# Optimization experiments

Hardware: AMD Instinct MI355X
Metric: run time of the kernel (lower is better)

The kernel has to match this reference:

```python
import jax, jax.numpy as jnp
import numpy as np

DIM = 96
DIM_OUT = 96
NUM_HEADS = 1
HEAD_DIM = DIM_OUT // NUM_HEADS  # 96, also depthwise-conv channel count
STRIDE_Q = 1
STRIDE_KV = 2
EPS = 1e-6


def _layernorm(t, g, b):
    mu = jnp.mean(t, axis=-1, keepdims=True)
    var = jnp.mean(jnp.square(t - mu), axis=-1, keepdims=True)
    return (t - mu) * jax.lax.rsqrt(var + EPS) * g + b


def _depthwise(t_nchw, w, stride):
    # torch Conv2d(C, C, 3, stride, padding=1, groups=C, bias=False)
    # w: [C, 1, 3, 3]
    return jax.lax.conv_general_dilated(
        t_nchw, w, window_strides=(stride, stride), padding=[(1, 1), (1, 1)],
        feature_group_count=HEAD_DIM, dimension_numbers=('NCHW', 'OIHW', 'NCHW'))


def _attention_pool(t, w, stride, g, b, H, W):
    # t: [B, heads, L, C] -> pooled [B, heads, Lp, C]
    B, nh, L, C = t.shape
    t = t.reshape(B * nh, H, W, C).transpose(0, 3, 1, 2)  # [B*nh, C, H, W]
    t = _depthwise(t, w, stride)
    Hp, Wp = t.shape[2], t.shape[3]
    t = t.reshape(B, nh, C, Hp * Wp).transpose(0, 1, 3, 2)  # [B, nh, Lp, C]
    return _layernorm(t, g, b), Hp, Wp


def setup_inputs() -> dict:
    key = jax.random.key(0)
    ks = jax.random.split(key, 16)
    B, N = 32, 56 * 56
    inp = {
        'x': jax.random.normal(ks[0], (B, N, DIM), dtype=jnp.float32),
        'Wqkv': jax.random.normal(ks[1], (3 * DIM_OUT, DIM), dtype=jnp.float32) * 0.02,
        'bqkv': jax.random.normal(ks[2], (3 * DIM_OUT,), dtype=jnp.float32) * 0.02,
        'pool_q_w': jax.random.normal(ks[3], (HEAD_DIM, 1, 3, 3), dtype=jnp.float32) * 0.1,
        'gq': 1.0 + jax.random.normal(ks[4], (HEAD_DIM,), dtype=jnp.float32) * 0.02,
        'betq': jax.random.normal(ks[5], (HEAD_DIM,), dtype=jnp.float32) * 0.02,
        'pool_k_w': jax.random.normal(ks[6], (HEAD_DIM, 1, 3, 3), dtype=jnp.float32) * 0.1,
        'gk': 1.0 + jax.random.normal(ks[7], (HEAD_DIM,), dtype=jnp.float32) * 0.02,
        'betk': jax.random.normal(ks[8], (HEAD_DIM,), dtype=jnp.float32) * 0.02,
        'pool_v_w': jax.random.normal(ks[9], (HEAD_DIM, 1, 3, 3), dtype=jnp.float32) * 0.1,
        'gv': 1.0 + jax.random.normal(ks[10], (HEAD_DIM,), dtype=jnp.float32) * 0.02,
        'betv': jax.random.normal(ks[11], (HEAD_DIM,), dtype=jnp.float32) * 0.02,
        'Wproj': jax.random.normal(ks[12], (DIM_OUT, DIM_OUT), dtype=jnp.float32) * 0.02,
        'bproj': jax.random.normal(ks[13], (DIM_OUT,), dtype=jnp.float32) * 0.02,
        'h': 56,
        'w': 56,
    }
    return inp


def reference(x, Wqkv, bqkv, pool_q_w, gq, betq, pool_k_w, gk, betk,
              pool_v_w, gv, betv, Wproj, bproj, h, w):
    B, N, _ = x.shape
    qkv = (jnp.einsum('bnd,ed->bne', x, Wqkv) + bqkv)
    qkv = qkv.reshape(B, N, 3, NUM_HEADS, HEAD_DIM).transpose(2, 0, 3, 1, 4)
    q, k, v = qkv[0], qkv[1], qkv[2]  # each [B, heads, N, head_dim]

    q, Hq, Wq = _attention_pool(q, pool_q_w, STRIDE_Q, gq, betq, h, w)
    k, _, _ = _attention_pool(k, pool_k_w, STRIDE_KV, gk, betk, h, w)
    v, _, _ = _attention_pool(v, pool_v_w, STRIDE_KV, gv, betv, h, w)

    scale = HEAD_DIM ** -0.5
    attn = jax.nn.softmax(jnp.einsum('bhqc,bhkc->bhqk', q * scale, k), axis=-1)
    out = jnp.einsum('bhqk,bhkc->bhqc', attn, v) + q  # residual x + q
    out = out.transpose(0, 2, 1, 3).reshape(B, Hq * Wq, DIM_OUT)
    out = jnp.einsum('bnd,ed->bne', out, Wproj) + bproj
    return out
```

## Files before the change

kernel.cpp:

```cpp
#include <hip/hip_runtime.h>
#include <hip/hip_bf16.h>
#include <cmath>

#define BATCH 32
#define H_IN 56
#define W_IN 56
#define N_IN (H_IN * W_IN)
#define LKV 784
#define LKV_PAD 864
#define FRAG_ELEMS 82944

typedef short bf16x8 __attribute__((ext_vector_type(8)));
typedef float f32x4 __attribute__((ext_vector_type(4)));
typedef float f32x16 __attribute__((ext_vector_type(16)));

__device__ __forceinline__ unsigned pack_bf16(float a, float b) {
    unsigned ua = __builtin_bit_cast(unsigned, a);
    unsigned ub = __builtin_bit_cast(unsigned, b);
    ua = (ua + 0x7FFFu + ((ua >> 16) & 1u)) >> 16;
    ub = (ub + 0x7FFFu + ((ub >> 16) & 1u)) >> 16;
    return ua | (ub << 16);
}

__device__ __forceinline__ unsigned short cvt_bf16(float a) {
    unsigned ua = __builtin_bit_cast(unsigned, a);
    return (unsigned short)((ua + 0x7FFFu + ((ua >> 16) & 1u)) >> 16);
}

__device__ __forceinline__ float bf16_to_f32(unsigned short u) {
    unsigned v = ((unsigned)u) << 16;
    return __builtin_bit_cast(float, v);
}

__device__ __forceinline__ float bflo(unsigned u) {
    return __builtin_bit_cast(float, u << 16);
}
__device__ __forceinline__ float bfhi(unsigned u) {
    return __builtin_bit_cast(float, u & 0xFFFF0000u);
}

__device__ __forceinline__ unsigned pack_trunc(float a, float b) {
    return __builtin_amdgcn_perm(__builtin_bit_cast(unsigned, b),
                                 __builtin_bit_cast(unsigned, a), 0x07060302u);
}

__device__ __forceinline__ f32x16 zero16() {
    f32x16 z;
#pragma unroll
    for (int i = 0; i < 16; ++i) z[i] = 0.f;
    return z;
}

__global__ __launch_bounds__(256) void wprep_kernel(
    const float* __restrict__ Wqkv, const float* __restrict__ Wproj,
    const float* __restrict__ pqw, const float* __restrict__ pkw,
    const float* __restrict__ pvw,
    unsigned short* __restrict__ wq, unsigned short* __restrict__ wp,
    float* __restrict__ wpool)
{
    int idx = blockIdx.x * 256 + threadIdx.x;
    if (idx < 4608) {
        const float* src; unsigned short* dst; int li;
        if (idx < 3456) { src = Wqkv; dst = wq; li = idx; }
        else            { src = Wproj; dst = wp; li = idx - 3456; }
        int frag = li >> 6, ln = li & 63;
        int ct = frag / 3, kkb = frag % 3;
        int ch = ct * 16 + (ln & 15);
        int k0 = kkb * 32 + (ln >> 4) * 8;
        const float* s = src + ch * 96 + k0;
        float4 v0 = *reinterpret_cast<const float4*>(s);
        float4 v1 = *reinterpret_cast<const float4*>(s + 4);
        uint4 o;
        o.x = pack_bf16(v0.x, v0.y); o.y = pack_bf16(v0.z, v0.w);
        o.z = pack_bf16(v1.x, v1.y); o.w = pack_bf16(v1.z, v1.w);
        *reinterpret_cast<uint4*>(dst + (size_t)li * 8) = o;
    } else if (idx < 7200) {
        int li = idx - 4608;
        int which = li / 864, r = li % 864;
        int tap = r / 96, c = r % 96;
        const float* src = (which == 0) ? pqw : (which == 1 ? pkw : pvw);
        wpool[which * 864 + tap * 96 + c] = src[c * 9 + tap];
    }
}

template <int NCT, bool IN_BF16, bool OUT_F32>
__global__ __launch_bounds__(256, 2) void gemm2_kernel(
    const void* __restrict__ Xv, const unsigned short* __restrict__ Wfr,
    const float* __restrict__ bias, void* __restrict__ o0,
    void* __restrict__ o1, void* __restrict__ o2)
{
    __shared__ unsigned short Wl[NCT * 192 * 8];
    const int tid = threadIdx.x;
    const int wid = tid >> 6, lane = tid & 63;
    const int lo16 = lane & 15, hi = lane >> 4;

    for (int idx = tid; idx < NCT * 192; idx += 256)
        *reinterpret_cast<int4*>(&Wl[idx * 8]) =
            *reinterpret_cast<const int4*>(Wfr + (size_t)idx * 8);

    const size_t tok0 = (size_t)blockIdx.x * 256 + wid * 64;
    bf16x8 xb[12];
#pragma unroll
    for (int it = 0; it < 4; ++it) {
        size_t t = tok0 + it * 16 + lo16;
#pragma unroll
        for (int kkb = 0; kkb < 3; ++kkb) {
            if constexpr (IN_BF16) {
                xb[it * 3 + kkb] = *reinterpret_cast<const bf16x8*>(
                    (const unsigned short*)Xv + t * 96 + kkb * 32 + hi * 8);
            } else {
                const float* xp = (const float*)Xv + t * 96 + kkb * 32 + hi * 8;
                float4 a = *reinterpret_cast<const float4*>(xp);
                float4 c = *reinterpret_cast<const float4*>(xp + 4);
                uint4 u;
                u.x = pack_bf16(a.x, a.y); u.y = pack_bf16(a.z, a.w);
                u.z = pack_bf16(c.x, c.y); u.w = pack_bf16(c.z, c.w);
                xb[it * 3 + kkb] = __builtin_bit_cast(bf16x8, u);
            }
        }
    }
    __syncthreads();

#pragma unroll
    for (int ct = 0; ct < NCT; ++ct) {
        bf16x8 wf[3];
#pragma unroll
        for (int kkb = 0; kkb < 3; ++kkb)
            wf[kkb] = *reinterpret_cast<const bf16x8*>(&Wl[((ct * 3 + kkb) * 64 + lane) * 8]);
        const int chb = ct * 16 + hi * 4;
        float4 bv = *reinterpret_cast<const float4*>(bias + chb);
#pragma unroll
        for (int it = 0; it < 4; ++it) {
            f32x4 a = (f32x4){0.f, 0.f, 0.f, 0.f};
#pragma unroll
            for (int kkb = 0; kkb < 3; ++kkb)
                a = __builtin_amdgcn_mfma_f32_16x16x32_bf16(wf[kkb], xb[it * 3 + kkb], a, 0, 0, 0);
            size_t t = tok0 + it * 16 + lo16;
            float r0 = a[0] + bv.x, r1 = a[1] + bv.y;
            float r2 = a[2] + bv.z, r3 = a[3] + bv.w;
            if constexpr (OUT_F32) {
                *reinterpret_cast<float4*>((float*)o0 + t * 96 + chb) =
                    make_float4(r0, r1, r2, r3);
            } else {
                unsigned short* ob =
                    (unsigned short*)((ct < 6) ? o0 : (ct < 12 ? o1 : o2));
                int lch = (ct % 6) * 16 + hi * 4;
                uint2 p;
                p.x = pack_bf16(r0, r1);
                p.y = pack_bf16(r2, r3);
                *reinterpret_cast<uint2*>(ob + t * 96 + lch) = p;
            }
        }
    }
}

template <int OMODE, int STRIDE>
__global__ __launch_bounds__(192) void pool_ln4_kernel(
    const unsigned short* __restrict__ in, const float* __restrict__ pwt,
    const float* __restrict__ g, const float* __restrict__ beta,
    unsigned short* __restrict__ out, int Hp, int Wp, int LpPad, float oscale)
{
    __shared__ float2 part[192];
    __shared__ float2 mrs[16];
    const int tid = threadIdx.x;
    const int tok_l = tid / 12, c8 = tid % 12;
    const int gt = blockIdx.x * 16 + tok_l;
    const int Lp = Hp * Wp;
    const int b = gt / LpPad, rem = gt % LpPad;
    const bool pad = (rem >= Lp);
    const int yo = rem / Wp, xo = rem % Wp;

    float wt[9][8];
#pragma unroll
    for (int tap = 0; tap < 9; ++tap) {
        float4 w0 = *reinterpret_cast<const float4*>(pwt + tap * 96 + c8 * 8);
        float4 w1 = *reinterpret_cast<const float4*>(pwt + tap * 96 + c8 * 8 + 4);
        wt[tap][0] = w0.x; wt[tap][1] = w0.y; wt[tap][2] = w0.z; wt[tap][3] = w0.w;
        wt[tap][4] = w1.x; wt[tap][5] = w1.y; wt[tap][6] = w1.z; wt[tap][7] = w1.w;
    }

    float acc[8];
#pragma unroll
    for (int j = 0; j < 8; ++j) acc[j] = 0.f;

    const unsigned short* ib = in + (size_t)b * (H_IN * W_IN * 96) + c8 * 8;
#pragma unroll
    for (int dy = 0; dy < 3; ++dy) {
        const int iy = yo * STRIDE + dy - 1;
        if ((unsigned)iy < (unsigned)H_IN) {
#pragma unroll
            for (int dx = 0; dx < 3; ++dx) {
                const int ix = xo * STRIDE + dx - 1;
                if ((unsigned)ix < (unsigned)W_IN) {
                    const int tap = dy * 3 + dx;
                    uint4 d = *reinterpret_cast<const uint4*>(
                        ib + ((size_t)iy * W_IN + ix) * 96);
                    acc[0] += bflo(d.x) * wt[tap][0];
                    acc[1] += bfhi(d.x) * wt[tap][1];
                    acc[2] += bflo(d.y) * wt[tap][2];
                    acc[3] += bfhi(d.y) * wt[tap][3];
                    acc[4] += bflo(d.z) * wt[tap][4];
                    acc[5] += bfhi(d.z) * wt[tap][5];
                    acc[6] += bflo(d.w) * wt[tap][6];
                    acc[7] += bfhi(d.w) * wt[tap][7];
                }
            }
        }
    }

    float s = 0.f, s2 = 0.f;
#pragma unroll
    for (int j = 0; j < 8; ++j) { s += acc[j]; s2 += acc[j] * acc[j]; }
    part[tid] = make_float2(s, s2);
    __syncthreads();
    if (tid < 16) {
        float a = 0.f, q = 0.f;
#pragma unroll
        for (int j = 0; j < 12; ++j) {
            float2 p = part[tid * 12 + j];
            a += p.x; q += p.y;
        }
        float mu = a * (1.f / 96.f);
        float var = q * (1.f / 96.f) - mu * mu;
        mrs[tid] = make_float2(mu, rsqrtf(var + 1e-6f));
    }
    __syncthreads();
    const float mu = mrs[tok_l].x, rstd = mrs[tok_l].y;

    float4 g0 = *reinterpret_cast<const float4*>(g + c8 * 8);
    float4 g1 = *reinterpret_cast<const float4*>(g + c8 * 8 + 4);
    float4 b0 = *reinterpret_cast<const float4*>(beta + c8 * 8);
    float4 b1 = *reinterpret_cast<const float4*>(beta + c8 * 8 + 4);
    float r[8];
    r[0] = (acc[0] - mu) * rstd * (g0.x * oscale) + b0.x * oscale;
    r[1] = (acc[1] - mu) * rstd * (g0.y * oscale) + b0.y * oscale;
    r[2] = (acc[2] - mu) * rstd * (g0.z * oscale) + b0.z * oscale;
    r[3] = (acc[3] - mu) * rstd * (g0.w * oscale) + b0.w * oscale;
    r[4] = (acc[4] - mu) * rstd * (g1.x * oscale) + b1.x * oscale;
    r[5] = (acc[5] - mu) * rstd * (g1.y * oscale) + b1.y * oscale;
    r[6] = (acc[6] - mu) * rstd * (g1.z * oscale) + b1.z * oscale;
    r[7] = (acc[7] - mu) * rstd * (g1.w * oscale) + b1.w * oscale;
    if (OMODE != 0 && pad) {
#pragma unroll
        for (int j = 0; j < 8; ++j) r[j] = 0.f;
    }

    if constexpr (OMODE == 0) {
        uint4 o;
        o.x = pack_bf16(r[0], r[1]); o.y = pack_bf16(r[2], r[3]);
        o.z = pack_bf16(r[4], r[5]); o.w = pack_bf16(r[6], r[7]);
        *reinterpret_cast<uint4*>(out + (size_t)gt * 96 + c8 * 8) = o;
    } else if constexpr (OMODE == 1) {
        int t = rem >> 5, kkb = c8 >> 1, hi = c8 & 1;
        int ln = (rem & 31) | (hi << 5);
        uint4 o;
        o.x = pack_bf16(r[0], r[1]); o.y = pack_bf16(r[2], r[3]);
        o.z = pack_bf16(r[4], r[5]); o.w = pack_bf16(r[6], r[7]);
        *reinterpret_cast<uint4*>(out + (size_t)b * FRAG_ELEMS +
                                  ((size_t)(t * 6 + kkb) * 64 + ln) * 8) = o;
    } else {
        int kv16 = rem >> 4, e = rem & 7, lh = (rem >> 3) & 1;
#pragma unroll
        for (int j = 0; j < 8; ++j) {
            int j8 = c8 * 8 + j;
            int ct = j8 >> 5;
            int ln = (j8 & 31) | (lh << 5);
            out[(size_t)b * FRAG_ELEMS + ((size_t)(kv16 * 3 + ct) * 64 + ln) * 8 + e] =
                cvt_bf16(r[j]);
        }
    }
}

#define ATT_LOAD(KF, V0, V1, T)                                               \
    {                                                                         \
        _Pragma("unroll") for (int i_ = 0; i_ < 6; ++i_)                      \
            KF[i_] = *reinterpret_cast<const bf16x8*>(                        \
                Kb + ((size_t)((T) * 6 + i_) * 64 + lane) * 8);               \
        _Pragma("unroll") for (int c_ = 0; c_ < 3; ++c_) {                    \
            V0[c_] = *reinterpret_cast<const bf16x8*>(                        \
                Vb + ((size_t)((2 * (T)) * 3 + c_) * 64 + lane) * 8);         \
            V1[c_] = *reinterpret_cast<const bf16x8*>(                        \
                Vb + ((size_t)((2 * (T) + 1) * 3 + c_) * 64 + lane) * 8);     \
        }                                                                     \
    }

#define ATT_COMPUTE(KF, V0, V1, FULL)                                         \
    {                                                                         \
        f32x16 s = zero16();                                                  \
        _Pragma("unroll") for (int k_ = 0; k_ < 6; ++k_)                      \
            s = __builtin_amdgcn_mfma_f32_32x32x16_bf16(KF[k_], qf[k_], s, 0, 0, 0); \
        float p[16];                                                          \
        _Pragma("unroll") for (int r_ = 0; r_ < 16; ++r_) {                   \
            float e_ = __builtin_amdgcn_exp2f(s[r_]);                         \
            p[r_] = __builtin_bit_cast(float,                                 \
                      __builtin_bit_cast(unsigned, e_) & 0xFFFF0000u);        \
        }                                                                     \
        float q0_ = 0.f, q1_ = 0.f;                                           \
        _Pragma("unroll") for (int r_ = 0; r_ < 8; ++r_) {                    \
            q0_ += p[r_]; q1_ += p[r_ + 8];                                   \
        }                                                                     \
        lsum += q0_ + ((FULL) ? q1_ : 0.f);                                   \
        unsigned d[8], sw[8];                                                 \
        _Pragma("unroll") for (int j_ = 0; j_ < 8; ++j_)                      \
            d[j_] = pack_trunc(p[2 * j_], p[2 * j_ + 1]);                     \
        _Pragma("unroll") for (int j_ = 0; j_ < 8; ++j_)                      \
            sw[j_] = (unsigned)__shfl_xor((int)d[j_], 32);                    \
        {                                                                     \
            int4 bi = h ? make_int4((int)sw[2], (int)sw[3], (int)d[2], (int)d[3]) \
                        : make_int4((int)d[0], (int)d[1], (int)sw[0], (int)sw[1]); \
            bf16x8 bf = __builtin_bit_cast(bf16x8, bi);                       \
            a0 = __builtin_amdgcn_mfma_f32_32x32x16_bf16(V0[0], bf, a0, 0, 0, 0); \
            a1 = __builtin_amdgcn_mfma_f32_32x32x16_bf16(V0[1], bf, a1, 0, 0, 0); \
            a2 = __builtin_amdgcn_mfma_f32_32x32x16_bf16(V0[2], bf, a2, 0, 0, 0); \
        }                                                                     \
        if (FULL) {                                                           \
            int4 bi = h ? make_int4((int)sw[6], (int)sw[7], (int)d[6], (int)d[7]) \
                        : make_int4((int)d[4], (int)d[5], (int)sw[4], (int)sw[5]); \
            bf16x8 bf = __builtin_bit_cast(bf16x8, bi);                       \
            a0 = __builtin_amdgcn_mfma_f32_32x32x16_bf16(V1[0], bf, a0, 0, 0, 0); \
            a1 = __builtin_amdgcn_mfma_f32_32x32x16_bf16(V1[1], bf, a1, 0, 0, 0); \
            a2 = __builtin_amdgcn_mfma_f32_32x32x16_bf16(V1[2], bf, a2, 0, 0, 0); \
        }                                                                     \
    }

__global__ __launch_bounds__(64) void attn_mfma7_kernel(
    const unsigned short* __restrict__ qpl, const unsigned short* __restrict__ Kf,
    const unsigned short* __restrict__ Vf, unsigned short* __restrict__ out)
{
    const int bid = blockIdx.x;
    const int swz = (bid & 7) * 392 + (bid >> 3);
    const int b = swz / 98, qblk = swz % 98;
    const int lane = threadIdx.x;
    const int l31 = lane & 31, h = lane >> 5;

    const int qrow = qblk * 32 + l31;
    const unsigned short* qptr = qpl + ((size_t)b * N_IN + qrow) * 96;
    bf16x8 qf[6];
#pragma unroll
    for (int kkb = 0; kkb < 6; ++kkb)
        qf[kkb] = *reinterpret_cast<const bf16x8*>(qptr + kkb * 16 + h * 8);

    f32x16 a0 = zero16(), a1 = zero16(), a2 = zero16();
    float lsum = 0.f;

    const unsigned short* Kb = Kf + (size_t)b * FRAG_ELEMS;
    const unsigned short* Vb = Vf + (size_t)b * FRAG_ELEMS;

    bf16x8 kA[6], vA0[3], vA1[3];
    bf16x8 kB[6], vB0[3], vB1[3];

    ATT_LOAD(kA, vA0, vA1, 0);
    for (int t = 0; t < 24; t += 2) {
        ATT_LOAD(kB, vB0, vB1, t + 1);
        ATT_COMPUTE(kA, vA0, vA1, true);
        ATT_LOAD(kA, vA0, vA1, t + 2);
        ATT_COMPUTE(kB, vB0, vB1, true);
    }
    ATT_COMPUTE(kA, vA0, vA1, false);

    lsum += __shfl_xor(lsum, 32);
    const float inv = 1.f / lsum;

    unsigned short* op = out + ((size_t)b * N_IN + qrow) * 96;
#pragma unroll
    for (int ct = 0; ct < 3; ++ct) {
        const f32x16& a = (ct == 0) ? a0 : (ct == 1 ? a1 : a2);
#pragma unroll
        for (int gblk = 0; gblk < 4; ++gblk) {
            int ch = ct * 32 + gblk * 8 + 4 * h;
            ushort4 q4 = *reinterpret_cast<const ushort4*>(qptr + ch);
            uint2 pr;
            pr.x = pack_bf16(a[gblk * 4 + 0] * inv + bf16_to_f32(q4.x),
                             a[gblk * 4 + 1] * inv + bf16_to_f32(q4.y));
            pr.y = pack_bf16(a[gblk * 4 + 2] * inv + bf16_to_f32(q4.z),
                             a[gblk * 4 + 3] * inv + bf16_to_f32(q4.w));
            *reinterpret_cast<uint2*>(op + ch) = pr;
        }
    }
}

extern "C" void kernel_launch(void* const* d_in, const int* in_sizes, int n_in,
                              void* d_out, int out_size, void* d_ws, size_t ws_size,
                              hipStream_t stream)
{
    const float* x     = (const float*)d_in[0];
    const float* Wqkv  = (const float*)d_in[1];
    const float* bqkv  = (const float*)d_in[2];
    const float* pqw   = (const float*)d_in[3];
    const float* gq    = (const float*)d_in[4];
    const float* betq  = (const float*)d_in[5];
    const float* pkw   = (const float*)d_in[6];
    const float* gk    = (const float*)d_in[7];
    const float* betk  = (const float*)d_in[8];
    const float* pvw   = (const float*)d_in[9];
    const float* gv    = (const float*)d_in[10];
    const float* betv  = (const float*)d_in[11];
    const float* Wproj = (const float*)d_in[12];
    const float* bproj = (const float*)d_in[13];
    float* outp = (float*)d_out;

    char* ws = (char*)d_ws;
    const size_t QB    = (size_t)BATCH * N_IN * 96 * sizeof(short);
    const size_t FRAGB = (size_t)BATCH * FRAG_ELEMS * sizeof(short);
    unsigned short* qb   = (unsigned short*)(ws);
    unsigned short* kbuf = (unsigned short*)(ws + QB);
    unsigned short* vbuf = (unsigned short*)(ws + 2 * QB);
    unsigned short* qpb  = (unsigned short*)(ws + 3 * QB);
    unsigned short* Kfr  = (unsigned short*)(ws + 4 * QB);
    unsigned short* Vfr  = (unsigned short*)(ws + 4 * QB + FRAGB);
    unsigned short* wqf  = (unsigned short*)(ws + 4 * QB + 2 * FRAGB);
    unsigned short* wpf  = (unsigned short*)(ws + 4 * QB + 2 * FRAGB + 56320);
    float*          wpool = (float*)(ws + 4 * QB + 2 * FRAGB + 56320 + 18432);
    unsigned short* attn_out = qb;

    const int T = BATCH * N_IN;

    const float SC = 0.1020620726159658f * 1.4426950408889634f;

    wprep_kernel<<<29, 256, 0, stream>>>(Wqkv, Wproj, pqw, pkw, pvw, wqf, wpf, wpool);
    gemm2_kernel<18, false, false><<<T / 256, 256, 0, stream>>>(
        x, wqf, bqkv, qb, kbuf, vbuf);
    pool_ln4_kernel<0, 1><<<T / 16, 192, 0, stream>>>(
        qb, wpool, gq, betq, qpb, 56, 56, N_IN, 1.0f);
    pool_ln4_kernel<1, 2><<<(BATCH * LKV_PAD) / 16, 192, 0, stream>>>(
        kbuf, wpool + 864, gk, betk, Kfr, 28, 28, LKV_PAD, SC);
    pool_ln4_kernel<2, 2><<<(BATCH * LKV_PAD) / 16, 192, 0, stream>>>(
        vbuf, wpool + 1728, gv, betv, Vfr, 28, 28, LKV_PAD, 1.0f);
    attn_mfma7_kernel<<<3136, 64, 0, stream>>>(qpb, Kfr, Vfr, attn_out);
    gemm2_kernel<6, true, true><<<T / 256, 256, 0, stream>>>(
        attn_out, wpf, bproj, outp, nullptr, nullptr);
}
```

Before: 151.0 us.

## Fold weight prep into GEMMs, merge pooling launches, regroup attention into 4-wave blocks

```diff
diff --git a/kernel.cpp b/kernel.cpp
--- a/kernel.cpp
+++ b/kernel.cpp
@@ -51,41 +51,9 @@
     return z;
 }
 
-__global__ __launch_bounds__(256) void wprep_kernel(
-    const float* __restrict__ Wqkv, const float* __restrict__ Wproj,
-    const float* __restrict__ pqw, const float* __restrict__ pkw,
-    const float* __restrict__ pvw,
-    unsigned short* __restrict__ wq, unsigned short* __restrict__ wp,
-    float* __restrict__ wpool)
-{
-    int idx = blockIdx.x * 256 + threadIdx.x;
-    if (idx < 4608) {
-        const float* src; unsigned short* dst; int li;
-        if (idx < 3456) { src = Wqkv; dst = wq; li = idx; }
-        else            { src = Wproj; dst = wp; li = idx - 3456; }
-        int frag = li >> 6, ln = li & 63;
-        int ct = frag / 3, kkb = frag % 3;
-        int ch = ct * 16 + (ln & 15);
-        int k0 = kkb * 32 + (ln >> 4) * 8;
-        const float* s = src + ch * 96 + k0;
-        float4 v0 = *reinterpret_cast<const float4*>(s);
-        float4 v1 = *reinterpret_cast<const float4*>(s + 4);
-        uint4 o;
-        o.x = pack_bf16(v0.x, v0.y); o.y = pack_bf16(v0.z, v0.w);
-        o.z = pack_bf16(v1.x, v1.y); o.w = pack_bf16(v1.z, v1.w);
-        *reinterpret_cast<uint4*>(dst + (size_t)li * 8) = o;
-    } else if (idx < 7200) {
-        int li = idx - 4608;
-        int which = li / 864, r = li % 864;
-        int tap = r / 96, c = r % 96;
-        const float* src = (which == 0) ? pqw : (which == 1 ? pkw : pvw);
-        wpool[which * 864 + tap * 96 + c] = src[c * 9 + tap];
-    }
-}
-
 template <int NCT, bool IN_BF16, bool OUT_F32>
-__global__ __launch_bounds__(256, 2) void gemm2_kernel(
-    const void* __restrict__ Xv, const unsigned short* __restrict__ Wfr,
+__global__ __launch_bounds__(256, 2) void gemm3_kernel(
+    const void* __restrict__ Xv, const float* __restrict__ W,
     const float* __restrict__ bias, void* __restrict__ o0,
     void* __restrict__ o1, void* __restrict__ o2)
 {
@@ -94,14 +62,24 @@
     const int wid = tid >> 6, lane = tid & 63;
     const int lo16 = lane & 15, hi = lane >> 4;
 
-    for (int idx = tid; idx < NCT * 192; idx += 256)
-        *reinterpret_cast<int4*>(&Wl[idx * 8]) =
-            *reinterpret_cast<const int4*>(Wfr + (size_t)idx * 8);
-
-    const size_t tok0 = (size_t)blockIdx.x * 256 + wid * 64;
-    bf16x8 xb[12];
-#pragma unroll
-    for (int it = 0; it < 4; ++it) {
+    for (int idx = tid; idx < NCT * 192; idx += 256) {
+        int frag = idx >> 6, ln = idx & 63;
+        int ct = frag / 3, kkb = frag % 3;
+        int ch = ct * 16 + (ln & 15);
+        int k0 = kkb * 32 + (ln >> 4) * 8;
+        const float* s = W + ch * 96 + k0;
+        float4 v0 = *reinterpret_cast<const float4*>(s);
+        float4 v1 = *reinterpret_cast<const float4*>(s + 4);
+        uint4 o;
+        o.x = pack_bf16(v0.x, v0.y); o.y = pack_bf16(v0.z, v0.w);
+        o.z = pack_bf16(v1.x, v1.y); o.w = pack_bf16(v1.z, v1.w);
+        *reinterpret_cast<uint4*>(&Wl[idx * 8]) = o;
+    }
+
+    const size_t tok0 = (size_t)blockIdx.x * 128 + wid * 32;
+    bf16x8 xb[6];
+#pragma unroll
+    for (int it = 0; it < 2; ++it) {
         size_t t = tok0 + it * 16 + lo16;
 #pragma unroll
         for (int kkb = 0; kkb < 3; ++kkb) {
@@ -130,7 +108,7 @@
         const int chb = ct * 16 + hi * 4;
         float4 bv = *reinterpret_cast<const float4*>(bias + chb);
 #pragma unroll
-        for (int it = 0; it < 4; ++it) {
+        for (int it = 0; it < 2; ++it) {
             f32x4 a = (f32x4){0.f, 0.f, 0.f, 0.f};
 #pragma unroll
             for (int kkb = 0; kkb < 3; ++kkb)
@@ -154,29 +132,56 @@
     }
 }
 
-template <int OMODE, int STRIDE>
-__global__ __launch_bounds__(192) void pool_ln4_kernel(
-    const unsigned short* __restrict__ in, const float* __restrict__ pwt,
-    const float* __restrict__ g, const float* __restrict__ beta,
-    unsigned short* __restrict__ out, int Hp, int Wp, int LpPad, float oscale)
+__global__ __launch_bounds__(192) void pool_all_kernel(
+    const unsigned short* __restrict__ qin, const unsigned short* __restrict__ kin,
+    const unsigned short* __restrict__ vin,
+    const float* __restrict__ pqw, const float* __restrict__ pkw,
+    const float* __restrict__ pvw,
+    const float* __restrict__ gq, const float* __restrict__ betq,
+    const float* __restrict__ gk, const float* __restrict__ betk,
+    const float* __restrict__ gv, const float* __restrict__ betv,
+    unsigned short* __restrict__ qout, unsigned short* __restrict__ kfr,
+    unsigned short* __restrict__ vfr, float SC)
 {
+    __shared__ float wlds[864];
     __shared__ float2 part[192];
     __shared__ float2 mrs[16];
+
+    int blk = blockIdx.x;
+    const unsigned short* in; const float* wsrc; const float* g; const float* beta;
+    unsigned short* out; int omode, stride, Wp, LpPad; float oscale;
+    if (blk < 6272) {
+        in = qin; wsrc = pqw; g = gq; beta = betq; out = qout;
+        omode = 0; stride = 1; Wp = 56; LpPad = N_IN; oscale = 1.0f;
+    } else if (blk < 8000) {
+        blk -= 6272;
+        in = kin; wsrc = pkw; g = gk; beta = betk; out = kfr;
+        omode = 1; stride = 2; Wp = 28; LpPad = LKV_PAD; oscale = SC;
+    } else {
+        blk -= 8000;
+        in = vin; wsrc = pvw; g = gv; beta = betv; out = vfr;
+        omode = 2; stride = 2; Wp = 28; LpPad = LKV_PAD; oscale = 1.0f;
+    }
+
     const int tid = threadIdx.x;
+    for (int i = tid; i < 216; i += 192)
+        *reinterpret_cast<float4*>(&wlds[i * 4]) =
+            *reinterpret_cast<const float4*>(wsrc + i * 4);
+    __syncthreads();
+
     const int tok_l = tid / 12, c8 = tid % 12;
-    const int gt = blockIdx.x * 16 + tok_l;
-    const int Lp = Hp * Wp;
+    const int gt = blk * 16 + tok_l;
+    const int Lp = (omode == 0) ? N_IN : LKV;
     const int b = gt / LpPad, rem = gt % LpPad;
     const bool pad = (rem >= Lp);
     const int yo = rem / Wp, xo = rem % Wp;
 
     float wt[9][8];
 #pragma unroll
-    for (int tap = 0; tap < 9; ++tap) {
-        float4 w0 = *reinterpret_cast<const float4*>(pwt + tap * 96 + c8 * 8);
-        float4 w1 = *reinterpret_cast<const float4*>(pwt + tap * 96 + c8 * 8 + 4);
-        wt[tap][0] = w0.x; wt[tap][1] = w0.y; wt[tap][2] = w0.z; wt[tap][3] = w0.w;
-        wt[tap][4] = w1.x; wt[tap][5] = w1.y; wt[tap][6] = w1.z; wt[tap][7] = w1.w;
+    for (int j = 0; j < 8; ++j) {
+        const float* wr = &wlds[(c8 * 8 + j) * 9];
+#pragma unroll
+        for (int tap = 0; tap < 9; ++tap) wt[tap][j] = wr[tap];
     }
 
     float acc[8];
@@ -186,11 +191,11 @@
     const unsigned short* ib = in + (size_t)b * (H_IN * W_IN * 96) + c8 * 8;
 #pragma unroll
     for (int dy = 0; dy < 3; ++dy) {
-        const int iy = yo * STRIDE + dy - 1;
+        const int iy = yo * stride + dy - 1;
         if ((unsigned)iy < (unsigned)H_IN) {
 #pragma unroll
             for (int dx = 0; dx < 3; ++dx) {
-                const int ix = xo * STRIDE + dx - 1;
+                const int ix = xo * stride + dx - 1;
                 if ((unsigned)ix < (unsigned)W_IN) {
                     const int tap = dy * 3 + dx;
                     uint4 d = *reinterpret_cast<const uint4*>(
@@ -240,17 +245,17 @@
     r[5] = (acc[5] - mu) * rstd * (g1.y * oscale) + b1.y * oscale;
     r[6] = (acc[6] - mu) * rstd * (g1.z * oscale) + b1.z * oscale;
     r[7] = (acc[7] - mu) * rstd * (g1.w * oscale) + b1.w * oscale;
-    if (OMODE != 0 && pad) {
+    if (omode != 0 && pad) {
 #pragma unroll
         for (int j = 0; j < 8; ++j) r[j] = 0.f;
     }
 
-    if constexpr (OMODE == 0) {
+    if (omode == 0) {
         uint4 o;
         o.x = pack_bf16(r[0], r[1]); o.y = pack_bf16(r[2], r[3]);
         o.z = pack_bf16(r[4], r[5]); o.w = pack_bf16(r[6], r[7]);
         *reinterpret_cast<uint4*>(out + (size_t)gt * 96 + c8 * 8) = o;
-    } else if constexpr (OMODE == 1) {
+    } else if (omode == 1) {
         int t = rem >> 5, kkb = c8 >> 1, hi = c8 & 1;
         int ln = (rem & 31) | (hi << 5);
         uint4 o;
@@ -286,15 +291,16 @@
 
 #define ATT_COMPUTE(KF, V0, V1, FULL)                                         \
     {                                                                         \
-        f32x16 s = zero16();                                                  \
-        _Pragma("unroll") for (int k_ = 0; k_ < 6; ++k_)                      \
-            s = __builtin_amdgcn_mfma_f32_32x32x16_bf16(KF[k_], qf[k_], s, 0, 0, 0); \
+        f32x16 sE = zero16(), sO = zero16();                                  \
+        sE = __builtin_amdgcn_mfma_f32_32x32x16_bf16(KF[0], qf[0], sE, 0, 0, 0); \
+        sO = __builtin_amdgcn_mfma_f32_32x32x16_bf16(KF[1], qf[1], sO, 0, 0, 0); \
+        sE = __builtin_amdgcn_mfma_f32_32x32x16_bf16(KF[2], qf[2], sE, 0, 0, 0); \
+        sO = __builtin_amdgcn_mfma_f32_32x32x16_bf16(KF[3], qf[3], sO, 0, 0, 0); \
+        sE = __builtin_amdgcn_mfma_f32_32x32x16_bf16(KF[4], qf[4], sE, 0, 0, 0); \
+        sO = __builtin_amdgcn_mfma_f32_32x32x16_bf16(KF[5], qf[5], sO, 0, 0, 0); \
         float p[16];                                                          \
-        _Pragma("unroll") for (int r_ = 0; r_ < 16; ++r_) {                   \
-            float e_ = __builtin_amdgcn_exp2f(s[r_]);                         \
-            p[r_] = __builtin_bit_cast(float,                                 \
-                      __builtin_bit_cast(unsigned, e_) & 0xFFFF0000u);        \
-        }                                                                     \
+        _Pragma("unroll") for (int r_ = 0; r_ < 16; ++r_)                     \
+            p[r_] = __builtin_amdgcn_exp2f(sE[r_] + sO[r_]);                  \
         float q0_ = 0.f, q1_ = 0.f;                                           \
         _Pragma("unroll") for (int r_ = 0; r_ < 8; ++r_) {                    \
             q0_ += p[r_]; q1_ += p[r_ + 8];                                   \
@@ -323,14 +329,16 @@
         }                                                                     \
     }
 
-__global__ __launch_bounds__(64) void attn_mfma7_kernel(
+__global__ __launch_bounds__(256) void attn_mfma8_kernel(
     const unsigned short* __restrict__ qpl, const unsigned short* __restrict__ Kf,
     const unsigned short* __restrict__ Vf, unsigned short* __restrict__ out)
 {
     const int bid = blockIdx.x;
-    const int swz = (bid & 7) * 392 + (bid >> 3);
-    const int b = swz / 98, qblk = swz % 98;
-    const int lane = threadIdx.x;
+    const int wid = threadIdx.x >> 6;
+    const int sblk = (bid & 7) * 98 + (bid >> 3);
+    const int unit = sblk * 4 + wid;
+    const int b = unit / 98, qblk = unit % 98;
+    const int lane = threadIdx.x & 63;
     const int l31 = lane & 31, h = lane >> 5;
 
     const int qrow = qblk * 32 + l31;
@@ -408,25 +416,18 @@
     unsigned short* qpb  = (unsigned short*)(ws + 3 * QB);
     unsigned short* Kfr  = (unsigned short*)(ws + 4 * QB);
     unsigned short* Vfr  = (unsigned short*)(ws + 4 * QB + FRAGB);
-    unsigned short* wqf  = (unsigned short*)(ws + 4 * QB + 2 * FRAGB);
-    unsigned short* wpf  = (unsigned short*)(ws + 4 * QB + 2 * FRAGB + 56320);
-    float*          wpool = (float*)(ws + 4 * QB + 2 * FRAGB + 56320 + 18432);
     unsigned short* attn_out = qb;
 
     const int T = BATCH * N_IN;
 
     const float SC = 0.1020620726159658f * 1.4426950408889634f;
 
-    wprep_kernel<<<29, 256, 0, stream>>>(Wqkv, Wproj, pqw, pkw, pvw, wqf, wpf, wpool);
-    gemm2_kernel<18, false, false><<<T / 256, 256, 0, stream>>>(
-        x, wqf, bqkv, qb, kbuf, vbuf);
-    pool_ln4_kernel<0, 1><<<T / 16, 192, 0, stream>>>(
-        qb, wpool, gq, betq, qpb, 56, 56, N_IN, 1.0f);
-    pool_ln4_kernel<1, 2><<<(BATCH * LKV_PAD) / 16, 192, 0, stream>>>(
-        kbuf, wpool + 864, gk, betk, Kfr, 28, 28, LKV_PAD, SC);
-    pool_ln4_kernel<2, 2><<<(BATCH * LKV_PAD) / 16, 192, 0, stream>>>(
-        vbuf, wpool + 1728, gv, betv, Vfr, 28, 28, LKV_PAD, 1.0f);
-    attn_mfma7_kernel<<<3136, 64, 0, stream>>>(qpb, Kfr, Vfr, attn_out);
-    gemm2_kernel<6, true, true><<<T / 256, 256, 0, stream>>>(
-        attn_out, wpf, bproj, outp, nullptr, nullptr);
-}
+    gemm3_kernel<18, false, false><<<T / 128, 256, 0, stream>>>(
+        x, Wqkv, bqkv, qb, kbuf, vbuf);
+    pool_all_kernel<<<9728, 192, 0, stream>>>(
+        qb, kbuf, vbuf, pqw, pkw, pvw, gq, betq, gk, betk, gv, betv,
+        qpb, Kfr, Vfr, SC);
+    attn_mfma8_kernel<<<784, 256, 0, stream>>>(qpb, Kfr, Vfr, attn_out);
+    gemm3_kernel<6, true, true><<<T / 128, 256, 0, stream>>>(
+        attn_out, Wproj, bproj, outp, nullptr, nullptr);
+}
```

After: 151.4 us. About the same (+0.2%).
